# Kernel optimization log

Measured on AMD Instinct MI355X. Metric: run time of the kernel, lower is better.

The kernel has to match this reference:

```python
import jax, jax.numpy as jnp
import numpy as np
import math

B, T, D = 2, 2048, 2048
H, HKV, HD = 16, 4, 128
THETA = 10000.0


def _rope_tables(seq_len, head_dim, theta):
    inv_freq = 1.0 / theta ** (jnp.arange(0, head_dim, 2, dtype=jnp.float32) / head_dim)
    t = jnp.arange(seq_len, dtype=jnp.float32)
    freqs = jnp.outer(t, inv_freq)  # (T, HD/2)
    return jnp.cos(freqs), jnp.sin(freqs)


def _apply_rope(x, cos, sin):
    # x: (B, h, T, HD); cos/sin: (T, HD/2)
    hd = x.shape[-1]
    x1, x2 = x[..., : hd // 2], x[..., hd // 2 :]
    rotated = jnp.concatenate([-x2, x1], axis=-1)
    c = jnp.concatenate([cos, cos], axis=-1)[None, None]  # (1,1,T,HD)
    s = jnp.concatenate([sin, sin], axis=-1)[None, None]
    return x * c + rotated * s


def setup_inputs() -> dict:
    key = jax.random.key(0)
    ks = jax.random.split(key, 5)
    sc = 0.02
    return {
        "x": jax.random.normal(ks[0], (B, T, D), dtype=jnp.float32),
        "attention_mask": jnp.ones((B, T), dtype=jnp.int32),
        "causal": 1,
        "wq": jax.random.normal(ks[1], (D, H * HD), dtype=jnp.float32) * sc,
        "wk": jax.random.normal(ks[2], (D, HKV * HD), dtype=jnp.float32) * sc,
        "wv": jax.random.normal(ks[3], (D, HKV * HD), dtype=jnp.float32) * sc,
        "wo": jax.random.normal(ks[4], (D, D), dtype=jnp.float32) * sc,
    }


def reference(x, attention_mask, causal, wq, wk, wv, wo):
    b, t, d = x.shape
    G = H // HKV  # query heads per kv head

    q = (x @ wq).reshape(b, t, H, HD).transpose(0, 2, 1, 3)      # (B,H,T,HD)
    k = (x @ wk).reshape(b, t, HKV, HD).transpose(0, 2, 1, 3)    # (B,HKV,T,HD)
    v = (x @ wv).reshape(b, t, HKV, HD).transpose(0, 2, 1, 3)

    cos, sin = _rope_tables(t, HD, THETA)
    q = _apply_rope(q, cos, sin)
    k = _apply_rope(k, cos, sin)

    # group queries so repeat_interleave of k/v is implicit
    qg = q.reshape(b, HKV, G, t, HD)
    scores = jnp.einsum("bkgtd,bksd->bkgts", qg, k) / math.sqrt(HD)

    key_pad = (attention_mask == 0)[:, None, None, None, :]  # (B,1,1,1,T)
    scores = jnp.where(key_pad, -jnp.inf, scores)
    if causal:
        cm = jnp.triu(jnp.ones((t, t), dtype=bool), k=1)
        scores = jnp.where(cm[None, None, None], -jnp.inf, scores)

    attn = jax.nn.softmax(scores, axis=-1)  # dropout p=0.0 -> identity in eval
    out = jnp.einsum("bkgts,bksd->bkgtd", attn, v)            # (B,HKV,G,T,HD)
    out = out.reshape(b, H, t, HD).transpose(0, 2, 1, 3).reshape(b, t, H * HD)
    return out @ wo
```

## Files before the change

kernel.cpp:

```cpp
#include <hip/hip_runtime.h>
#include <hip/hip_bf16.h>
#include <stdint.h>

#define B_    2
#define T_    2048
#define D_    2048
#define H_    16
#define HKV_  4
#define HD_   128
#define BT_   (B_ * T_)
#define QD_   2048
#define KVD_  512

typedef float  f32x4 __attribute__((ext_vector_type(4)));
typedef short  s16x8 __attribute__((ext_vector_type(8)));
typedef unsigned short us;

__device__ __forceinline__ us f2bf(float f) {
    unsigned int u = __builtin_bit_cast(unsigned int, f);
    u += 0x7FFFu + ((u >> 16) & 1u);
    return (us)(u >> 16);
}
__device__ __forceinline__ float bf2f(us s) {
    unsigned int u = ((unsigned int)s) << 16;
    return __builtin_bit_cast(float, u);
}
__device__ __forceinline__ unsigned pack2(float a, float b) {
    return (unsigned)f2bf(a) | ((unsigned)f2bf(b) << 16);
}

#define GLOBAL_AS __attribute__((address_space(1)))
#define LDS_AS    __attribute__((address_space(3)))

__device__ __forceinline__ void gload16(const void* g, void* l) {
    __builtin_amdgcn_global_load_lds((const GLOBAL_AS uint32_t*)g,
                                     (LDS_AS uint32_t*)l, 16, 0, 0);
}

__global__ __launch_bounds__(256)
void wtrans(const float* __restrict__ w, us* __restrict__ wt, int K, int N) {
    __shared__ float t[32][33];
    const int k0 = blockIdx.x * 32, n0 = blockIdx.y * 32;
    const int tid = threadIdx.x;
    const int r = tid >> 3, c4 = (tid & 7) << 2;
    const float4 v = *(const float4*)&w[(size_t)(k0 + r) * N + n0 + c4];
    t[r][c4 + 0] = v.x; t[r][c4 + 1] = v.y; t[r][c4 + 2] = v.z; t[r][c4 + 3] = v.w;
    __syncthreads();
    ushort4 o;
    o.x = f2bf(t[c4 + 0][r]); o.y = f2bf(t[c4 + 1][r]);
    o.z = f2bf(t[c4 + 2][r]); o.w = f2bf(t[c4 + 3][r]);
    *(ushort4*)&wt[(size_t)(n0 + r) * K + k0 + c4] = o;
}

__global__ __launch_bounds__(256)
void cvt_bf16(const float* __restrict__ x, us* __restrict__ xb, int n8) {
    const int i = blockIdx.x * 256 + threadIdx.x;
    if (i >= n8) return;
    const float4 a = ((const float4*)x)[i * 2];
    const float4 b = ((const float4*)x)[i * 2 + 1];
    s16x8 o;
    o[0] = (short)f2bf(a.x); o[1] = (short)f2bf(a.y);
    o[2] = (short)f2bf(a.z); o[3] = (short)f2bf(a.w);
    o[4] = (short)f2bf(b.x); o[5] = (short)f2bf(b.y);
    o[6] = (short)f2bf(b.z); o[7] = (short)f2bf(b.w);
    *(s16x8*)&xb[(size_t)i * 8] = o;
}

__global__ __launch_bounds__(256)
void build_tabs(float* __restrict__ tab, float* __restrict__ bias,
                const int* __restrict__ amask) {
    const int i = blockIdx.x * 256 + threadIdx.x;
    if (i < T_ * 64) {
        const int t = i >> 6, f = i & 63;
        const float inv = __expf((float)f * (-0.14391156642478335f));
        float s, c;
        sincosf((float)t * inv, &s, &c);
        tab[t * 128 + f] = c;
        tab[t * 128 + 64 + f] = s;
    }
    if (i < B_ * T_) bias[i] = amask[i] ? 0.f : -__builtin_inff();
}

template <int NH>
__global__ __launch_bounds__(256)
void rope_apply(us* __restrict__ x, const float* __restrict__ tab, int total4) {
    const int idx = blockIdx.x * 256 + threadIdx.x;
    if (idx >= total4) return;
    const int i0  = (idx & 15) << 2;
    const int rest = idx >> 4;
    const int h   = rest % NH;
    const int row = rest / NH;
    const int t   = row & (T_ - 1);
    const f32x4 c = *(const f32x4*)&tab[t * 128 + i0];
    const f32x4 s = *(const f32x4*)&tab[t * 128 + 64 + i0];
    const size_t base = (size_t)row * (NH * 128) + h * 128 + i0;
    ushort4 lo = *(ushort4*)&x[base];
    ushort4 hi = *(ushort4*)&x[base + 64];
    float x1[4] = {bf2f(lo.x), bf2f(lo.y), bf2f(lo.z), bf2f(lo.w)};
    float x2[4] = {bf2f(hi.x), bf2f(hi.y), bf2f(hi.z), bf2f(hi.w)};
    ushort4 olo, ohi;
    olo.x = f2bf(x1[0]*c[0] - x2[0]*s[0]); ohi.x = f2bf(x2[0]*c[0] + x1[0]*s[0]);
    olo.y = f2bf(x1[1]*c[1] - x2[1]*s[1]); ohi.y = f2bf(x2[1]*c[1] + x1[1]*s[1]);
    olo.z = f2bf(x1[2]*c[2] - x2[2]*s[2]); ohi.z = f2bf(x2[2]*c[2] + x1[2]*s[2]);
    olo.w = f2bf(x1[3]*c[3] - x2[3]*s[3]); ohi.w = f2bf(x2[3]*c[3] + x1[3]*s[3]);
    *(ushort4*)&x[base]      = olo;
    *(ushort4*)&x[base + 64] = ohi;
}

template <bool AF32, int OUTMODE>
__global__ __launch_bounds__(256)
void gemm_bf16(const void* __restrict__ Ap, const us* __restrict__ Bt,
               void* __restrict__ Cp, int M, int N, int K) {
    __shared__ us As[128 * 32];
    __shared__ us Bs[128 * 32];

    const int tid  = threadIdx.x;
    const int lane = tid & 63;
    const int w    = tid >> 6;
    const int lrow = lane & 15;
    const int lhi  = lane >> 4;
    const int wm   = w >> 1;
    const int wn   = w & 1;
    const int mbase = blockIdx.y * 128;
    const int nbase = blockIdx.x * 128;

    f32x4 acc[4][4] = {};

    for (int k0 = 0; k0 < K; k0 += 32) {
        __syncthreads();
        if constexpr (AF32) {
            const float* A = (const float*)Ap;
#pragma unroll
            for (int i = 0; i < 2; ++i) {
                const int c   = tid * 2 + i;
                const int row = c >> 2, cc = c & 3;
                const float* src = A + (size_t)(mbase + row) * K + k0 + ((cc ^ (row & 3)) << 3);
                const float4 v0 = *(const float4*)src;
                const float4 v1 = *(const float4*)(src + 4);
                s16x8 o;
                o[0] = (short)f2bf(v0.x); o[1] = (short)f2bf(v0.y);
                o[2] = (short)f2bf(v0.z); o[3] = (short)f2bf(v0.w);
                o[4] = (short)f2bf(v1.x); o[5] = (short)f2bf(v1.y);
                o[6] = (short)f2bf(v1.z); o[7] = (short)f2bf(v1.w);
                *(s16x8*)&As[c * 8] = o;
            }
        } else {
            const us* A = (const us*)Ap;
#pragma unroll
            for (int i = 0; i < 2; ++i) {
                const int cb = i * 256 + w * 64;
                const int c  = cb + lane;
                const int row = c >> 2, cc = c & 3;
                gload16(A + (size_t)(mbase + row) * K + k0 + ((cc ^ (row & 3)) << 3),
                        &As[cb * 8]);
            }
        }
#pragma unroll
        for (int i = 0; i < 2; ++i) {
            const int cb = i * 256 + w * 64;
            const int c  = cb + lane;
            const int row = c >> 2, cc = c & 3;
            gload16(Bt + (size_t)(nbase + row) * K + k0 + ((cc ^ (row & 3)) << 3),
                    &Bs[cb * 8]);
        }
        __syncthreads();

        s16x8 af[4], bfv[4];
#pragma unroll
        for (int mi = 0; mi < 4; ++mi) {
            const int r = wm * 64 + mi * 16 + lrow;
            af[mi] = *(const s16x8*)&As[r * 32 + ((lhi ^ (r & 3)) << 3)];
        }
#pragma unroll
        for (int ni = 0; ni < 4; ++ni) {
            const int r = wn * 64 + ni * 16 + lrow;
            bfv[ni] = *(const s16x8*)&Bs[r * 32 + ((lhi ^ (r & 3)) << 3)];
        }
#pragma unroll
        for (int mi = 0; mi < 4; ++mi)
#pragma unroll
            for (int ni = 0; ni < 4; ++ni)
                acc[mi][ni] = __builtin_amdgcn_mfma_f32_16x16x32_bf16(
                    af[mi], bfv[ni], acc[mi][ni], 0, 0, 0);
    }

#pragma unroll
    for (int mi = 0; mi < 4; ++mi) {
#pragma unroll
        for (int ni = 0; ni < 4; ++ni) {
#pragma unroll
            for (int r = 0; r < 4; ++r) {
                const int gm = mbase + wm * 64 + mi * 16 + lhi * 4 + r;
                const int gn = nbase + wn * 64 + ni * 16 + lrow;
                const float v = acc[mi][ni][r];
                if constexpr (OUTMODE == 0) {
                    ((us*)Cp)[(size_t)gm * N + gn] = f2bf(v);
                } else if constexpr (OUTMODE == 1) {
                    ((float*)Cp)[(size_t)gm * N + gn] = v;
                } else {
                    const int b = gm >> 11, t = gm & (T_ - 1);
                    if (gn < KVD_) {
                        ((us*)Cp)[(size_t)gm * KVD_ + gn] = f2bf(v);
                    } else {
                        const int nv = gn - KVD_;
                        us* vt = (us*)Cp + (size_t)BT_ * KVD_;
                        vt[((size_t)(b * HKV_ + (nv >> 7)) * 128 + (nv & 127)) * T_ + t] = f2bf(v);
                    }
                }
            }
        }
    }
}

__global__ __launch_bounds__(256)
void attn_mfma2(const us* __restrict__ qg, const us* __restrict__ kg,
                const us* __restrict__ vtg, const float* __restrict__ bias,
                const int* __restrict__ causal_p, us* __restrict__ outg) {
    __shared__ us lds[32768];

    const int q0 = blockIdx.x * 64;
    const int h  = blockIdx.y;
    const int b  = blockIdx.z;
    const int kvh = h >> 2;
    const int causal = *causal_p;
    const int tid  = threadIdx.x;
    const int lane = tid & 63;
    const int w    = tid >> 6;
    const int lrow = lane & 15, lhi = lane >> 4;

    auto stageKV = [&](int buf, int s0) {
        us* Kd = lds + buf * 8192;
        us* Vd = lds + 16384 + buf * 8192;
#pragma unroll
        for (int i = 0; i < 4; ++i) {
            const int cb = i * 256 + w * 64;
            const int c  = cb + lane;
            const int row = c >> 4, cc = c & 15;
            gload16(kg + (size_t)(b * T_ + s0 + row) * KVD_ + kvh * HD_ + ((cc ^ (row & 7)) << 3),
                    Kd + cb * 8);
        }
#pragma unroll
        for (int i = 0; i < 4; ++i) {
            const int cb = i * 256 + w * 64;
            const int c  = cb + lane;
            const int row = c >> 3, cc = c & 7;
            gload16(vtg + (size_t)((b * HKV_ + kvh) * 128 + row) * T_ + s0 + ((cc ^ (row & 7)) << 3),
                    Vd + cb * 8);
        }
    };

#pragma unroll
    for (int i = 0; i < 4; ++i) {
        const int cb = i * 256 + w * 64;
        const int c  = cb + lane;
        const int row = c >> 4, cc = c & 15;
        gload16(qg + (size_t)(b * T_ + q0 + row) * QD_ + h * HD_ + ((cc ^ (row & 7)) << 3),
                lds + 8192 + cb * 8);
    }
    __syncthreads();

    s16x8 qf[4];
    {
        const us* Qsp = lds + 8192;
        const int qr = w * 16 + lrow;
#pragma unroll
        for (int kc = 0; kc < 4; ++kc)
            qf[kc] = *(const s16x8*)&Qsp[qr * 128 + (((kc * 4 + lhi) ^ (qr & 7)) << 3)];
    }
    stageKV(0, 0);
    __syncthreads();

    f32x4 o[8] = {};
    float m_run = -__builtin_inff();
    float l_run = 0.f;
    const int qp = q0 + w * 16 + lrow;
    const int smax = causal ? (q0 + 64) : T_;
    const int ntiles = smax >> 6;
    const float rscale = 0.08838834764831845f;
    int cur = 0;

    for (int it = 0; it < ntiles; ++it) {
        const int s0 = it << 6;
        if (it + 1 < ntiles) stageKV(cur ^ 1, s0 + 64);

        const us* Kcur = lds + cur * 8192;
        const us* Vcur = lds + 16384 + cur * 8192;

        f32x4 sf[4];
#pragma unroll
        for (int j = 0; j < 4; ++j) {
            f32x4 s = {0.f, 0.f, 0.f, 0.f};
            const int kr = j * 16 + lrow;
#pragma unroll
            for (int kc = 0; kc < 4; ++kc) {
                const s16x8 kf = *(const s16x8*)&Kcur[kr * 128 + (((kc * 4 + lhi) ^ (kr & 7)) << 3)];
                s = __builtin_amdgcn_mfma_f32_16x16x32_bf16(kf, qf[kc], s, 0, 0, 0);
            }
            sf[j] = s;
        }

        const float* brow = bias + b * T_ + s0;
        f32x4 bv[4];
#pragma unroll
        for (int j = 0; j < 4; ++j)
            bv[j] = *(const f32x4*)&brow[j * 16 + lhi * 4];
        const bool needc = causal && (s0 + 63 > q0 + w * 16);
        float x[4][4];
#pragma unroll
        for (int j = 0; j < 4; ++j)
#pragma unroll
            for (int r = 0; r < 4; ++r) {
                float xv = sf[j][r] * rscale + bv[j][r];
                if (needc && (s0 + j * 16 + lhi * 4 + r > qp)) xv = -__builtin_inff();
                x[j][r] = xv;
            }

        float tmax = x[0][0];
#pragma unroll
        for (int j = 0; j < 4; ++j)
#pragma unroll
            for (int r = 0; r < 4; ++r) tmax = fmaxf(tmax, x[j][r]);
        tmax = fmaxf(tmax, __shfl_xor(tmax, 16));
        tmax = fmaxf(tmax, __shfl_xor(tmax, 32));
        const float mn = fmaxf(m_run, tmax);
        float corr, ls = 0.f, ps[4][4];
        if (mn == -__builtin_inff()) {
            corr = 1.f;
#pragma unroll
            for (int j = 0; j < 4; ++j)
#pragma unroll
                for (int r = 0; r < 4; ++r) ps[j][r] = 0.f;
        } else {
            corr = __expf(m_run - mn);
#pragma unroll
            for (int j = 0; j < 4; ++j)
#pragma unroll
                for (int r = 0; r < 4; ++r) { ps[j][r] = __expf(x[j][r] - mn); ls += ps[j][r]; }
        }
        ls += __shfl_xor(ls, 16);
        ls += __shfl_xor(ls, 32);
        l_run = l_run * corr + ls;
        m_run = mn;

        const unsigned w00 = pack2(ps[0][0], ps[0][1]), w01 = pack2(ps[0][2], ps[0][3]);
        const unsigned w10 = pack2(ps[1][0], ps[1][1]), w11 = pack2(ps[1][2], ps[1][3]);
        const unsigned w20 = pack2(ps[2][0], ps[2][1]), w21 = pack2(ps[2][2], ps[2][3]);
        const unsigned w30 = pack2(ps[3][0], ps[3][1]), w31 = pack2(ps[3][2], ps[3][3]);
        int a0w[4], a1w[4];
#pragma unroll
        for (int m = 0; m < 4; ++m) {
            const int src = lrow + ((lhi & 1) << 5) + ((m & 2) << 3);
            const unsigned c0 = (m & 1) ? w01 : w00;
            const unsigned c1 = (m & 1) ? w11 : w10;
            const int t0 = __shfl((int)c0, src);
            const int t1 = __shfl((int)c1, src);
            a0w[m] = (lhi & 2) ? t1 : t0;
            const unsigned c2 = (m & 1) ? w21 : w20;
            const unsigned c3 = (m & 1) ? w31 : w30;
            const int t2 = __shfl((int)c2, src);
            const int t3 = __shfl((int)c3, src);
            a1w[m] = (lhi & 2) ? t3 : t2;
        }
        const s16x8 a0 = __builtin_bit_cast(s16x8, make_int4(a0w[0], a0w[1], a0w[2], a0w[3]));
        const s16x8 a1 = __builtin_bit_cast(s16x8, make_int4(a1w[0], a1w[1], a1w[2], a1w[3]));

        float co[4];
#pragma unroll
        for (int r = 0; r < 4; ++r) co[r] = __shfl(corr, lhi * 4 + r);
#pragma unroll
        for (int dc = 0; dc < 8; ++dc) {
            o[dc][0] *= co[0]; o[dc][1] *= co[1];
            o[dc][2] *= co[2]; o[dc][3] *= co[3];
        }
#pragma unroll
        for (int dc = 0; dc < 8; ++dc) {
            const int vr = dc * 16 + lrow;
            const s16x8 vb0 = *(const s16x8*)&Vcur[vr * 64 + ((lhi ^ (vr & 7)) << 3)];
            o[dc] = __builtin_amdgcn_mfma_f32_16x16x32_bf16(a0, vb0, o[dc], 0, 0, 0);
            const s16x8 vb1 = *(const s16x8*)&Vcur[vr * 64 + (((4 + lhi) ^ (vr & 7)) << 3)];
            o[dc] = __builtin_amdgcn_mfma_f32_16x16x32_bf16(a1, vb1, o[dc], 0, 0, 0);
        }
        __syncthreads();
        cur ^= 1;
    }

    float lq[4];
#pragma unroll
    for (int r = 0; r < 4; ++r) lq[r] = __shfl(l_run, lhi * 4 + r);
#pragma unroll
    for (int r = 0; r < 4; ++r) {
        const float invl = lq[r] > 0.f ? 1.0f / lq[r] : 0.f;
        const size_t base = (size_t)(b * T_ + q0 + w * 16 + lhi * 4 + r) * QD_ + h * HD_ + lrow;
#pragma unroll
        for (int dc = 0; dc < 8; ++dc)
            outg[base + dc * 16] = f2bf(o[dc][r] * invl);
    }
}

extern "C" void kernel_launch(void* const* d_in, const int* in_sizes, int n_in,
                              void* d_out, int out_size, void* d_ws, size_t ws_size,
                              hipStream_t stream) {
    const float* x      = (const float*)d_in[0];
    const int*   amask  = (const int*)d_in[1];
    const int*   causal = (const int*)d_in[2];
    const float* wq     = (const float*)d_in[3];
    const float* wk     = (const float*)d_in[4];
    const float* wv     = (const float*)d_in[5];
    const float* wo     = (const float*)d_in[6];
    float* out = (float*)d_out;

    us* p    = (us*)d_ws;
    us* wqt  = p;  p += (size_t)QD_ * D_;
    us* wkvt = p;  p += (size_t)1024 * D_;
    us* qb   = p;  p += (size_t)BT_ * QD_;
    us* kb   = p;  p += (size_t)BT_ * KVD_;
    us* vt   = p;  p += (size_t)BT_ * KVD_;
    float* tab  = (float*)p;  p += (size_t)T_ * 128 * 2;
    float* bias = (float*)p;  p += (size_t)B_ * T_ * 2;
    us* xw   = p;

    const size_t need_xb = ((size_t)(p - (us*)d_ws) + (size_t)BT_ * D_) * sizeof(us);
    const bool useXB = ws_size >= need_xb;

    build_tabs<<<512, 256, 0, stream>>>(tab, bias, amask);
    wtrans<<<dim3(64, 64), 256, 0, stream>>>(wq, wqt, D_, QD_);
    wtrans<<<dim3(64, 16), 256, 0, stream>>>(wk, wkvt, D_, KVD_);
    wtrans<<<dim3(64, 16), 256, 0, stream>>>(wv, wkvt + (size_t)KVD_ * D_, D_, KVD_);

    if (useXB) {
        cvt_bf16<<<4096, 256, 0, stream>>>(x, xw, BT_ * D_ / 8);
        gemm_bf16<false, 0><<<dim3(16, 32), 256, 0, stream>>>(xw, wqt, qb, BT_, QD_, D_);
        gemm_bf16<false, 2><<<dim3(8, 32), 256, 0, stream>>>(xw, wkvt, kb, BT_, 1024, D_);
    } else {
        gemm_bf16<true, 0><<<dim3(16, 32), 256, 0, stream>>>(x, wqt, qb, BT_, QD_, D_);
        gemm_bf16<true, 2><<<dim3(8, 32), 256, 0, stream>>>(x, wkvt, kb, BT_, 1024, D_);
    }

    rope_apply<H_><<<4096, 256, 0, stream>>>(qb, tab, BT_ * H_ * 16);
    rope_apply<HKV_><<<1024, 256, 0, stream>>>(kb, tab, BT_ * HKV_ * 16);

    attn_mfma2<<<dim3(32, 16, 2), 256, 0, stream>>>(qb, kb, vt, bias, causal, qb);

    wtrans<<<dim3(64, 64), 256, 0, stream>>>(wo, xw, D_, D_);
    gemm_bf16<false, 1><<<dim3(16, 32), 256, 0, stream>>>(qb, xw, out, BT_, D_, D_);
}
```

Measured before the change: 458.2 us.

## Swizzle GEMM blocks, vectorize V store, restructure attention V staging and softmax rescale

The GEMM remaps workgroup IDs in an XCD-aware order, raises wave priority around MFMA bursts, and writes the transposed V output as 4-wide vectors instead of scalar scattered stores. The attention kernel launches the longest causal tiles first, stages V through registers into a single LDS buffer so LDS use drops, and skips rescaling the output accumulator when the new tile max stays within a threshold of the running max. Together these target cache locality, store efficiency, load imbalance and softmax overhead. The cost is an extra barrier per tile and a lazy-rescale path that depends on the exponent bound staying numerically safe.

```diff
diff --git a/kernel.cpp b/kernel.cpp
--- a/kernel.cpp
+++ b/kernel.cpp
@@ -121,8 +121,13 @@
     const int lhi  = lane >> 4;
     const int wm   = w >> 1;
     const int wn   = w & 1;
-    const int mbase = blockIdx.y * 128;
-    const int nbase = blockIdx.x * 128;
+
+    const int gx  = gridDim.x;
+    const int nwg = gx * gridDim.y;
+    int lin = blockIdx.x + blockIdx.y * gx;
+    lin = (lin & 7) * (nwg >> 3) + (lin >> 3);
+    const int mbase = (lin / gx) * 128;
+    const int nbase = (lin % gx) * 128;
 
     f32x4 acc[4][4] = {};
 
@@ -176,36 +181,43 @@
             const int r = wn * 64 + ni * 16 + lrow;
             bfv[ni] = *(const s16x8*)&Bs[r * 32 + ((lhi ^ (r & 3)) << 3)];
         }
+        __builtin_amdgcn_s_setprio(1);
 #pragma unroll
         for (int mi = 0; mi < 4; ++mi)
 #pragma unroll
             for (int ni = 0; ni < 4; ++ni)
                 acc[mi][ni] = __builtin_amdgcn_mfma_f32_16x16x32_bf16(
                     af[mi], bfv[ni], acc[mi][ni], 0, 0, 0);
+        __builtin_amdgcn_s_setprio(0);
     }
 
 #pragma unroll
     for (int mi = 0; mi < 4; ++mi) {
 #pragma unroll
         for (int ni = 0; ni < 4; ++ni) {
-#pragma unroll
-            for (int r = 0; r < 4; ++r) {
-                const int gm = mbase + wm * 64 + mi * 16 + lhi * 4 + r;
-                const int gn = nbase + wn * 64 + ni * 16 + lrow;
-                const float v = acc[mi][ni][r];
-                if constexpr (OUTMODE == 0) {
-                    ((us*)Cp)[(size_t)gm * N + gn] = f2bf(v);
-                } else if constexpr (OUTMODE == 1) {
-                    ((float*)Cp)[(size_t)gm * N + gn] = v;
+            const int gm0 = mbase + wm * 64 + mi * 16 + lhi * 4;
+            const int gn  = nbase + wn * 64 + ni * 16 + lrow;
+            if constexpr (OUTMODE == 0) {
+#pragma unroll
+                for (int r = 0; r < 4; ++r)
+                    ((us*)Cp)[(size_t)(gm0 + r) * N + gn] = f2bf(acc[mi][ni][r]);
+            } else if constexpr (OUTMODE == 1) {
+#pragma unroll
+                for (int r = 0; r < 4; ++r)
+                    ((float*)Cp)[(size_t)(gm0 + r) * N + gn] = acc[mi][ni][r];
+            } else {
+                if (gn < KVD_) {
+#pragma unroll
+                    for (int r = 0; r < 4; ++r)
+                        ((us*)Cp)[(size_t)(gm0 + r) * KVD_ + gn] = f2bf(acc[mi][ni][r]);
                 } else {
-                    const int b = gm >> 11, t = gm & (T_ - 1);
-                    if (gn < KVD_) {
-                        ((us*)Cp)[(size_t)gm * KVD_ + gn] = f2bf(v);
-                    } else {
-                        const int nv = gn - KVD_;
-                        us* vt = (us*)Cp + (size_t)BT_ * KVD_;
-                        vt[((size_t)(b * HKV_ + (nv >> 7)) * 128 + (nv & 127)) * T_ + t] = f2bf(v);
-                    }
+                    const int nv = gn - KVD_;
+                    const int bb = gm0 >> 11, t = gm0 & (T_ - 1);
+                    us* vt = (us*)Cp + (size_t)BT_ * KVD_;
+                    ushort4 o4;
+                    o4.x = f2bf(acc[mi][ni][0]); o4.y = f2bf(acc[mi][ni][1]);
+                    o4.z = f2bf(acc[mi][ni][2]); o4.w = f2bf(acc[mi][ni][3]);
+                    *(ushort4*)&vt[((size_t)(bb * HKV_ + (nv >> 7)) * 128 + (nv & 127)) * T_ + t] = o4;
                 }
             }
         }
@@ -213,12 +225,13 @@
 }
 
 __global__ __launch_bounds__(256)
-void attn_mfma2(const us* __restrict__ qg, const us* __restrict__ kg,
+void attn_mfma4(const us* __restrict__ qg, const us* __restrict__ kg,
                 const us* __restrict__ vtg, const float* __restrict__ bias,
                 const int* __restrict__ causal_p, us* __restrict__ outg) {
-    __shared__ us lds[32768];
-
-    const int q0 = blockIdx.x * 64;
+    __shared__ us lds[24576];
+
+    const int qt = 31 - blockIdx.x;
+    const int q0 = qt * 64;
     const int h  = blockIdx.y;
     const int b  = blockIdx.z;
     const int kvh = h >> 2;
@@ -228,9 +241,8 @@
     const int w    = tid >> 6;
     const int lrow = lane & 15, lhi = lane >> 4;
 
-    auto stageKV = [&](int buf, int s0) {
+    auto stageK = [&](int buf, int s0) {
         us* Kd = lds + buf * 8192;
-        us* Vd = lds + 16384 + buf * 8192;
 #pragma unroll
         for (int i = 0; i < 4; ++i) {
             const int cb = i * 256 + w * 64;
@@ -239,13 +251,22 @@
             gload16(kg + (size_t)(b * T_ + s0 + row) * KVD_ + kvh * HD_ + ((cc ^ (row & 7)) << 3),
                     Kd + cb * 8);
         }
+    };
+    auto loadV = [&](s16x8 vr[4], int s0) {
 #pragma unroll
         for (int i = 0; i < 4; ++i) {
-            const int cb = i * 256 + w * 64;
-            const int c  = cb + lane;
+            const int c  = i * 256 + w * 64 + lane;
             const int row = c >> 3, cc = c & 7;
-            gload16(vtg + (size_t)((b * HKV_ + kvh) * 128 + row) * T_ + s0 + ((cc ^ (row & 7)) << 3),
-                    Vd + cb * 8);
+            vr[i] = *(const s16x8*)(vtg +
+                (size_t)((b * HKV_ + kvh) * 128 + row) * T_ + s0 + ((cc ^ (row & 7)) << 3));
+        }
+    };
+    auto writeV = [&](const s16x8 vr[4]) {
+        us* Vd = lds + 16384;
+#pragma unroll
+        for (int i = 0; i < 4; ++i) {
+            const int c = i * 256 + w * 64 + lane;
+            *(s16x8*)&Vd[c * 8] = vr[i];
         }
     };
 
@@ -267,26 +288,31 @@
         for (int kc = 0; kc < 4; ++kc)
             qf[kc] = *(const s16x8*)&Qsp[qr * 128 + (((kc * 4 + lhi) ^ (qr & 7)) << 3)];
     }
-    stageKV(0, 0);
+    s16x8 vreg[4];
+    stageK(0, 0);
+    loadV(vreg, 0);
+    __syncthreads();
+    writeV(vreg);
     __syncthreads();
 
     f32x4 o[8] = {};
     float m_run = -__builtin_inff();
     float l_run = 0.f;
     const int qp = q0 + w * 16 + lrow;
-    const int smax = causal ? (q0 + 64) : T_;
-    const int ntiles = smax >> 6;
+    const int ntiles = (causal ? (q0 + 64) : T_) >> 6;
     const float rscale = 0.08838834764831845f;
     int cur = 0;
 
     for (int it = 0; it < ntiles; ++it) {
         const int s0 = it << 6;
-        if (it + 1 < ntiles) stageKV(cur ^ 1, s0 + 64);
+        const bool more = (it + 1 < ntiles);
+        if (more) { stageK(cur ^ 1, s0 + 64); loadV(vreg, s0 + 64); }
 
         const us* Kcur = lds + cur * 8192;
-        const us* Vcur = lds + 16384 + cur * 8192;
+        const us* Vcur = lds + 16384;
 
         f32x4 sf[4];
+        __builtin_amdgcn_s_setprio(1);
 #pragma unroll
         for (int j = 0; j < 4; ++j) {
             f32x4 s = {0.f, 0.f, 0.f, 0.f};
@@ -298,6 +324,7 @@
             }
             sf[j] = s;
         }
+        __builtin_amdgcn_s_setprio(0);
 
         const float* brow = bias + b * T_ + s0;
         f32x4 bv[4];
@@ -322,25 +349,43 @@
             for (int r = 0; r < 4; ++r) tmax = fmaxf(tmax, x[j][r]);
         tmax = fmaxf(tmax, __shfl_xor(tmax, 16));
         tmax = fmaxf(tmax, __shfl_xor(tmax, 32));
-        const float mn = fmaxf(m_run, tmax);
-        float corr, ls = 0.f, ps[4][4];
-        if (mn == -__builtin_inff()) {
-            corr = 1.f;
+
+        const bool defer = (m_run != -__builtin_inff()) &&
+                           __all(tmax <= m_run + 8.f);
+        float corr = 1.f, ls = 0.f, ps[4][4];
+        if (defer) {
+            const float mo = m_run;
 #pragma unroll
             for (int j = 0; j < 4; ++j)
 #pragma unroll
-                for (int r = 0; r < 4; ++r) ps[j][r] = 0.f;
+                for (int r = 0; r < 4; ++r) { ps[j][r] = __expf(x[j][r] - mo); ls += ps[j][r]; }
         } else {
-            corr = __expf(m_run - mn);
-#pragma unroll
-            for (int j = 0; j < 4; ++j)
-#pragma unroll
-                for (int r = 0; r < 4; ++r) { ps[j][r] = __expf(x[j][r] - mn); ls += ps[j][r]; }
+            const float mn = fmaxf(m_run, tmax);
+            if (mn == -__builtin_inff()) {
+#pragma unroll
+                for (int j = 0; j < 4; ++j)
+#pragma unroll
+                    for (int r = 0; r < 4; ++r) ps[j][r] = 0.f;
+            } else {
+                corr = __expf(m_run - mn);
+#pragma unroll
+                for (int j = 0; j < 4; ++j)
+#pragma unroll
+                    for (int r = 0; r < 4; ++r) { ps[j][r] = __expf(x[j][r] - mn); ls += ps[j][r]; }
+            }
+            float co[4];
+#pragma unroll
+            for (int r = 0; r < 4; ++r) co[r] = __shfl(corr, lhi * 4 + r);
+#pragma unroll
+            for (int dc = 0; dc < 8; ++dc) {
+                o[dc][0] *= co[0]; o[dc][1] *= co[1];
+                o[dc][2] *= co[2]; o[dc][3] *= co[3];
+            }
+            m_run = mn;
         }
         ls += __shfl_xor(ls, 16);
         ls += __shfl_xor(ls, 32);
         l_run = l_run * corr + ls;
-        m_run = mn;
 
         const unsigned w00 = pack2(ps[0][0], ps[0][1]), w01 = pack2(ps[0][2], ps[0][3]);
         const unsigned w10 = pack2(ps[1][0], ps[1][1]), w11 = pack2(ps[1][2], ps[1][3]);
@@ -364,14 +409,7 @@
         const s16x8 a0 = __builtin_bit_cast(s16x8, make_int4(a0w[0], a0w[1], a0w[2], a0w[3]));
         const s16x8 a1 = __builtin_bit_cast(s16x8, make_int4(a1w[0], a1w[1], a1w[2], a1w[3]));
 
-        float co[4];
-#pragma unroll
-        for (int r = 0; r < 4; ++r) co[r] = __shfl(corr, lhi * 4 + r);
-#pragma unroll
-        for (int dc = 0; dc < 8; ++dc) {
-            o[dc][0] *= co[0]; o[dc][1] *= co[1];
-            o[dc][2] *= co[2]; o[dc][3] *= co[3];
-        }
+        __builtin_amdgcn_s_setprio(1);
 #pragma unroll
         for (int dc = 0; dc < 8; ++dc) {
             const int vr = dc * 16 + lrow;
@@ -380,6 +418,10 @@
             const s16x8 vb1 = *(const s16x8*)&Vcur[vr * 64 + (((4 + lhi) ^ (vr & 7)) << 3)];
             o[dc] = __builtin_amdgcn_mfma_f32_16x16x32_bf16(a1, vb1, o[dc], 0, 0, 0);
         }
+        __builtin_amdgcn_s_setprio(0);
+
+        __syncthreads();
+        if (more) writeV(vreg);
         __syncthreads();
         cur ^= 1;
     }
@@ -439,7 +481,7 @@
     rope_apply<H_><<<4096, 256, 0, stream>>>(qb, tab, BT_ * H_ * 16);
     rope_apply<HKV_><<<1024, 256, 0, stream>>>(kb, tab, BT_ * HKV_ * 16);
 
-    attn_mfma2<<<dim3(32, 16, 2), 256, 0, stream>>>(qb, kb, vt, bias, causal, qb);
+    attn_mfma4<<<dim3(32, 16, 2), 256, 0, stream>>>(qb, kb, vt, bias, causal, qb);
 
     wtrans<<<dim3(64, 64), 256, 0, stream>>>(wo, xw, D_, D_);
     gemm_bf16<false, 1><<<dim3(16, 32), 256, 0, stream>>>(qb, xw, out, BT_, D_, D_);
```

Result: faster. 440.0 us (-4.0%).
